# Kernel optimization log

Hardware: AMD Instinct MI355X
Metric: run time of the kernel (lower is better)

The kernel has to match this reference:

```python
import jax, jax.numpy as jnp
import numpy as np

B, S, E, H, D, F = 384, 128, 512, 4, 128, 2048

def setup_inputs() -> dict:
    key = jax.random.key(0)
    ks = jax.random.split(key, 13)
    lecun = lambda k, fan_in, shape: jax.random.normal(k, shape, jnp.float32) / jnp.sqrt(fan_in)
    return {
        "x": jax.random.normal(ks[0], (B, S, E), jnp.float32),
        "wq": lecun(ks[1], E, (E, E)), "bq": jnp.zeros((E,), jnp.float32),
        "wk": lecun(ks[2], E, (E, E)), "bk": jnp.zeros((E,), jnp.float32),
        "wv": lecun(ks[3], E, (E, E)), "bv": jnp.zeros((E,), jnp.float32),
        "wo": lecun(ks[4], E, (E, E)), "bo": jnp.zeros((E,), jnp.float32),
        "w1": lecun(ks[5], E, (E, F)), "b1": jnp.zeros((F,), jnp.float32),
        "w2": lecun(ks[6], F, (F, E)), "b2": jnp.zeros((E,), jnp.float32),
    }

def reference(x, wq, bq, wk, bk, wv, bv, wo, bo, w1, b1, w2, b2):
    # Attention (no 1/sqrt(d) scaling, no causal mask — matches source)
    q = (x @ wq + bq).reshape(B, S, H, D)
    k = (x @ wk + bk).reshape(B, S, H, D)
    v = (x @ wv + bv).reshape(B, S, H, D)
    scores = jnp.einsum('bshd,bthd->bhst', q, k)  # [B,H,S,S]
    weights = jax.nn.softmax(scores, axis=-1)
    attn = jnp.einsum('bhst,bthd->bshd', weights, v).reshape(B, S, E)
    x = x + (attn @ wo + bo)
    # MLP with residual
    h = jax.nn.relu(x @ w1 + b1)
    x = x + (h @ w2 + b2)
    return x
```

## Files before the change

kernel.cpp:

```cpp
#include <hip/hip_runtime.h>
#include <hip/hip_bf16.h>
#include <stdint.h>

typedef unsigned short u16;
typedef _Float16 f16;
typedef __attribute__((ext_vector_type(8))) f16 f16x8;
typedef __attribute__((ext_vector_type(4))) float f32x4;
typedef __attribute__((ext_vector_type(8))) u16 u16x8;

__device__ __forceinline__ u16 f2h(float f) {
    return __builtin_bit_cast(u16, (f16)f);
}
__device__ __forceinline__ float h2f(u16 u) {
    return (float)__builtin_bit_cast(f16, u);
}

#define GLDS16(g, l) __builtin_amdgcn_global_load_lds( \
    (const __attribute__((address_space(1))) void*)(uintptr_t)(g), \
    (__attribute__((address_space(3))) void*)(uintptr_t)(l), 16, 0, 0)

__global__ __launch_bounds__(256) void transpose_w(
    const float* __restrict__ in, u16* __restrict__ out,
    int K, int N, int rowOff)
{
    __shared__ float tile[32][33];
    int n0 = blockIdx.x * 32;
    int k0 = blockIdx.y * 32;
    int tx = threadIdx.x & 31;
    int ty = threadIdx.x >> 5;
#pragma unroll
    for (int i = 0; i < 4; ++i) {
        int k = ty + i * 8;
        tile[k][tx] = in[(size_t)(k0 + k) * N + n0 + tx];
    }
    __syncthreads();
#pragma unroll
    for (int i = 0; i < 4; ++i) {
        int n = ty + i * 8;
        out[(size_t)(rowOff + n0 + n) * K + k0 + tx] = f2h(tile[tx][n]);
    }
}

__global__ __launch_bounds__(256) void transpose_w4(
    const float* __restrict__ wq, const float* __restrict__ wk,
    const float* __restrict__ wv, const float* __restrict__ wo,
    u16* __restrict__ wqkvT, u16* __restrict__ woT)
{
    __shared__ float tile[32][33];
    const float* src[4] = {wq, wk, wv, wo};
    const int z = blockIdx.z;
    const float* in = src[z];
    u16* out = (z == 3) ? woT : (wqkvT + (size_t)z * 512 * 512);
    int n0 = blockIdx.x * 32;
    int k0 = blockIdx.y * 32;
    int tx = threadIdx.x & 31;
    int ty = threadIdx.x >> 5;
#pragma unroll
    for (int i = 0; i < 4; ++i) {
        int k = ty + i * 8;
        tile[k][tx] = in[(size_t)(k0 + k) * 512 + n0 + tx];
    }
    __syncthreads();
#pragma unroll
    for (int i = 0; i < 4; ++i) {
        int n = ty + i * 8;
        out[(size_t)(n0 + n) * 512 + k0 + tx] = f2h(tile[tx][n]);
    }
}

__global__ void pack_bias3(const float* __restrict__ bq, const float* __restrict__ bk,
                           const float* __restrict__ bv, float* __restrict__ bqkv)
{
    int i = blockIdx.x * 256 + threadIdx.x;
    float v;
    if (i < 512) v = bq[i];
    else if (i < 1024) v = bk[i - 512];
    else v = bv[i - 1024];
    bqkv[i] = v;
}

__global__ __launch_bounds__(256) void convert_x(const float* __restrict__ in,
                                                 u16* __restrict__ out)
{
    size_t i = ((size_t)blockIdx.x * 256 + threadIdx.x) * 8;
    float4 a = *(const float4*)(in + i);
    float4 b = *(const float4*)(in + i + 4);
    u16x8 r;
    r[0] = f2h(a.x); r[1] = f2h(a.y); r[2] = f2h(a.z); r[3] = f2h(a.w);
    r[4] = f2h(b.x); r[5] = f2h(b.y); r[6] = f2h(b.z); r[7] = f2h(b.w);
    *(u16x8*)(out + i) = r;
}

template<int RES, bool RELU, bool WH, bool WF32>
__global__ __launch_bounds__(256, 2) void gemm_bt(
    const u16* __restrict__ A, int lda,
    const u16* __restrict__ BT, int ldb,
    const float* __restrict__ bias, const float* __restrict__ res,
    u16* __restrict__ outh, float* __restrict__ outf,
    int nb_n, int N, int K)
{
    __shared__ u16 As[128 * 64];
    __shared__ u16 Bs[128 * 64];
    const int tid  = threadIdx.x;
    const int lane = tid & 63;
    const int wv   = tid >> 6;
    const int nwg  = gridDim.x;
    const int cpx  = nwg >> 3;
    const int logical = (blockIdx.x & 7) * cpx + (blockIdx.x >> 3);
    const int m0   = (logical / nb_n) * 128;
    const int n0   = (logical % nb_n) * 128;
    const int wm   = (wv >> 1) * 64;
    const int wn   = (wv & 1) * 64;
    const int lhi  = lane >> 4;
    const int llo  = lane & 15;

    f32x4 acc[4][4] = {};

    for (int kt = 0; kt < K; kt += 64) {
        __syncthreads();
#pragma unroll
        for (int i = 0; i < 4; ++i) {
            int c = i * 256 + tid;
            int row = c >> 3;
            int chunk = (c & 7) ^ (row & 7);
            const u16* ga = A  + (size_t)(m0 + row) * lda + kt + chunk * 8;
            const u16* gb = BT + (size_t)(n0 + row) * ldb + kt + chunk * 8;
            char* la = (char*)As + ((i * 256 + wv * 64) << 4);
            char* lb = (char*)Bs + ((i * 256 + wv * 64) << 4);
            GLDS16(ga, la);
            GLDS16(gb, lb);
        }
        __syncthreads();
#pragma unroll
        for (int fk = 0; fk < 2; ++fk) {
            f16x8 af[4], bfr[4];
#pragma unroll
            for (int f = 0; f < 4; ++f) {
                int ra = wm + f * 16 + llo;
                af[f] = *(const f16x8*)((const char*)As +
                        ((ra << 7) + ((fk * 64 + (lhi << 4)) ^ ((ra & 7) << 4))));
                int rb = wn + f * 16 + llo;
                bfr[f] = *(const f16x8*)((const char*)Bs +
                        ((rb << 7) + ((fk * 64 + (lhi << 4)) ^ ((rb & 7) << 4))));
            }
#pragma unroll
            for (int fm = 0; fm < 4; ++fm)
#pragma unroll
                for (int fn = 0; fn < 4; ++fn)
                    acc[fm][fn] = __builtin_amdgcn_mfma_f32_16x16x32_f16(
                        af[fm], bfr[fn], acc[fm][fn], 0, 0, 0);
        }
    }

    const int cr = lhi * 4;
#pragma unroll
    for (int fm = 0; fm < 4; ++fm) {
#pragma unroll
        for (int fn = 0; fn < 4; ++fn) {
            const int col = n0 + wn + fn * 16 + llo;
            const float bia = bias[col];
#pragma unroll
            for (int r = 0; r < 4; ++r) {
                const int row = m0 + wm + fm * 16 + cr + r;
                float v = acc[fm][fn][r] + bia;
                if constexpr (RES) v += res[(size_t)row * N + col];
                if constexpr (RELU) v = fmaxf(v, 0.f);
                if constexpr (WF32) outf[(size_t)row * N + col] = v;
                if constexpr (WH)   outh[(size_t)row * N + col] = f2h(v);
            }
        }
    }
}

__global__ __launch_bounds__(256, 2) void attn_kernel(
    const u16* __restrict__ qkv, u16* __restrict__ attn)
{
    __shared__ u16 VT[128 * 128];
    __shared__ u16 Plds[4 * 32 * 128];
    const int tid  = threadIdx.x;
    const int lane = tid & 63;
    const int wv   = tid >> 6;
    const int b    = blockIdx.x >> 2;
    const int hh   = blockIdx.x & 3;
    const int lhi  = lane >> 4;
    const int llo  = lane & 15;
    const u16* base = qkv + (size_t)b * 128 * 1536;

#pragma unroll
    for (int i = 0; i < 8; ++i) {
        int c = i * 256 + tid;
        int t = c >> 4;
        int ch = c & 15;
        uint4 raw = *(const uint4*)(base + (size_t)t * 1536 + 1024 + hh * 128 + ch * 8);
        const u16* e = (const u16*)&raw;
#pragma unroll
        for (int j = 0; j < 8; ++j) {
            int d = ch * 8 + j;
            *(u16*)((char*)VT + ((d << 8) + ((t * 2) ^ ((d & 7) << 4)))) = e[j];
        }
    }

    f16x8 qf[2][4];
#pragma unroll
    for (int fm = 0; fm < 2; ++fm)
#pragma unroll
        for (int fk = 0; fk < 4; ++fk) {
            int srow = wv * 32 + fm * 16 + llo;
            qf[fm][fk] = *(const f16x8*)(base + (size_t)srow * 1536 + hh * 128 + fk * 32 + lhi * 8);
        }

    f32x4 acc[2][8] = {};
#pragma unroll
    for (int ft = 0; ft < 8; ++ft) {
        f16x8 kf[4];
#pragma unroll
        for (int fk = 0; fk < 4; ++fk) {
            int trow = ft * 16 + llo;
            kf[fk] = *(const f16x8*)(base + (size_t)trow * 1536 + 512 + hh * 128 + fk * 32 + lhi * 8);
        }
#pragma unroll
        for (int fm = 0; fm < 2; ++fm)
#pragma unroll
            for (int fk = 0; fk < 4; ++fk)
                acc[fm][ft] = __builtin_amdgcn_mfma_f32_16x16x32_f16(
                    qf[fm][fk], kf[fk], acc[fm][ft], 0, 0, 0);
    }

    float inv[2][4];
#pragma unroll
    for (int fm = 0; fm < 2; ++fm)
#pragma unroll
        for (int r = 0; r < 4; ++r) {
            float mx = acc[fm][0][r];
#pragma unroll
            for (int ft = 1; ft < 8; ++ft) mx = fmaxf(mx, acc[fm][ft][r]);
            mx = fmaxf(mx, __shfl_xor(mx, 1, 64));
            mx = fmaxf(mx, __shfl_xor(mx, 2, 64));
            mx = fmaxf(mx, __shfl_xor(mx, 4, 64));
            mx = fmaxf(mx, __shfl_xor(mx, 8, 64));
            float s = 0.f;
#pragma unroll
            for (int ft = 0; ft < 8; ++ft) {
                float p = __expf(acc[fm][ft][r] - mx);
                acc[fm][ft][r] = p;
                s += p;
            }
            s += __shfl_xor(s, 1, 64);
            s += __shfl_xor(s, 2, 64);
            s += __shfl_xor(s, 4, 64);
            s += __shfl_xor(s, 8, 64);
            inv[fm][r] = 1.f / s;
        }

    char* Pw = (char*)Plds + wv * 8192;
#pragma unroll
    for (int fm = 0; fm < 2; ++fm)
#pragma unroll
        for (int ft = 0; ft < 8; ++ft)
#pragma unroll
            for (int r = 0; r < 4; ++r) {
                int m = fm * 16 + lhi * 4 + r;
                int t = ft * 16 + llo;
                *(u16*)(Pw + ((m << 8) + ((t * 2) ^ ((m & 7) << 4)))) = f2h(acc[fm][ft][r]);
            }

    __syncthreads();

    f16x8 pf[2][4];
#pragma unroll
    for (int fm = 0; fm < 2; ++fm)
#pragma unroll
        for (int k2 = 0; k2 < 4; ++k2) {
            int m = fm * 16 + llo;
            pf[fm][k2] = *(const f16x8*)(Pw +
                ((m << 8) + ((k2 * 64 + (lhi << 4)) ^ ((m & 7) << 4))));
        }

    f32x4 o[2][8] = {};
#pragma unroll
    for (int fd = 0; fd < 8; ++fd) {
        f16x8 vf[4];
#pragma unroll
        for (int k2 = 0; k2 < 4; ++k2) {
            int d = fd * 16 + llo;
            vf[k2] = *(const f16x8*)((const char*)VT +
                ((d << 8) + ((k2 * 64 + (lhi << 4)) ^ ((d & 7) << 4))));
        }
#pragma unroll
        for (int fm = 0; fm < 2; ++fm)
#pragma unroll
            for (int k2 = 0; k2 < 4; ++k2)
                o[fm][fd] = __builtin_amdgcn_mfma_f32_16x16x32_f16(
                    pf[fm][k2], vf[k2], o[fm][fd], 0, 0, 0);
    }

#pragma unroll
    for (int fm = 0; fm < 2; ++fm)
#pragma unroll
        for (int fd = 0; fd < 8; ++fd)
#pragma unroll
            for (int r = 0; r < 4; ++r) {
                int row = b * 128 + wv * 32 + fm * 16 + lhi * 4 + r;
                int col = hh * 128 + fd * 16 + llo;
                attn[(size_t)row * 512 + col] = f2h(o[fm][fd][r] * inv[fm][r]);
            }
}

extern "C" void kernel_launch(void* const* d_in, const int* in_sizes, int n_in,
                              void* d_out, int out_size, void* d_ws, size_t ws_size,
                              hipStream_t stream)
{
    const float* x  = (const float*)d_in[0];
    const float* wq = (const float*)d_in[1];
    const float* bq = (const float*)d_in[2];
    const float* wk = (const float*)d_in[3];
    const float* bk = (const float*)d_in[4];
    const float* wv = (const float*)d_in[5];
    const float* bv = (const float*)d_in[6];
    const float* wo = (const float*)d_in[7];
    const float* bo = (const float*)d_in[8];
    const float* w1 = (const float*)d_in[9];
    const float* b1 = (const float*)d_in[10];
    const float* w2 = (const float*)d_in[11];
    const float* b2 = (const float*)d_in[12];
    float* out = (float*)d_out;

    char* ws = (char*)d_ws;
    u16*   wqkvT = (u16*)(ws + 0);
    u16*   woT   = (u16*)(ws + 1572864);
    u16*   w1T   = (u16*)(ws + 2097152);
    u16*   w2T   = (u16*)(ws + 4194304);
    float* bqkv  = (float*)(ws + 6291456);
    u16*   xf    = (u16*)(ws + 6297600);
    u16*   qkv   = (u16*)(ws + 56629248);
    u16*   attno = xf;
    u16*   x1h   = qkv;
    u16*   hbuf  = (u16*)(ws + 106960896);
    float* x1f   = (float*)d_out;

    transpose_w4<<<dim3(16, 16, 4), 256, 0, stream>>>(wq, wk, wv, wo, wqkvT, woT);
    transpose_w<<<dim3(64, 16), 256, 0, stream>>>(w1, w1T, 512, 2048, 0);
    transpose_w<<<dim3(16, 64), 256, 0, stream>>>(w2, w2T, 2048, 512, 0);
    pack_bias3<<<6, 256, 0, stream>>>(bq, bk, bv, bqkv);
    convert_x<<<12288, 256, 0, stream>>>(x, xf);

    gemm_bt<0, false, true, false><<<4608, 256, 0, stream>>>(
        xf, 512, wqkvT, 512, bqkv, nullptr, qkv, nullptr, 12, 1536, 512);
    attn_kernel<<<1536, 256, 0, stream>>>(qkv, attno);
    gemm_bt<1, false, true, true><<<1536, 256, 0, stream>>>(
        attno, 512, woT, 512, bo, x, x1h, x1f, 4, 512, 512);
    gemm_bt<0, true, true, false><<<6144, 256, 0, stream>>>(
        x1h, 512, w1T, 512, b1, nullptr, hbuf, nullptr, 16, 2048, 512);
    gemm_bt<1, false, false, true><<<1536, 256, 0, stream>>>(
        hbuf, 2048, w2T, 2048, b2, x1f, nullptr, out, 4, 512, 2048);
}
```

Before: 512.9 us.

## Replace 128x128 GEMM with 256x256 eight-wave ping-pong pipelined GEMM

Swaps the 128x128-tile, 4-wave GEMM for a 256x256-tile, 8-wave kernel. It double-buffers A and B in 128KB of LDS and prefetches the next K-tiles with global_load_lds while MFMAs run on the current tile. The MFMA work is split into four quadrant phases, each with raised wave priority and explicit barriers and waitcnts, so LDS reads, global loads and matrix math interleave. Larger tiles improve operand reuse and cut global traffic. In exchange, occupancy drops to about one block per CU, the manual scheduling is fragile, and grids become small for the N=512 GEMMs (384 blocks).

```diff
diff --git a/kernel.cpp b/kernel.cpp
--- a/kernel.cpp
+++ b/kernel.cpp
@@ -11,13 +11,16 @@
 __device__ __forceinline__ u16 f2h(float f) {
     return __builtin_bit_cast(u16, (f16)f);
 }
-__device__ __forceinline__ float h2f(u16 u) {
-    return (float)__builtin_bit_cast(f16, u);
-}
 
 #define GLDS16(g, l) __builtin_amdgcn_global_load_lds( \
     (const __attribute__((address_space(1))) void*)(uintptr_t)(g), \
     (__attribute__((address_space(3))) void*)(uintptr_t)(l), 16, 0, 0)
+
+#define WAITL() do { asm volatile("s_waitcnt lgkmcnt(0)" ::: "memory"); \
+                     __builtin_amdgcn_sched_barrier(0); } while (0)
+#define BARR()  do { __builtin_amdgcn_sched_barrier(0); \
+                     __builtin_amdgcn_s_barrier(); \
+                     __builtin_amdgcn_sched_barrier(0); } while (0)
 
 __global__ __launch_bounds__(256) void transpose_w(
     const float* __restrict__ in, u16* __restrict__ out,
@@ -91,78 +94,149 @@
     *(u16x8*)(out + i) = r;
 }
 
+template<int MG, int NG>
+__device__ __forceinline__ void mmaQ(f32x4 (&acc)[8][4], const f16x8 (&a)[4][2],
+                                     const f16x8 (&bb)[2][2])
+{
+    __builtin_amdgcn_s_setprio(1);
+#pragma unroll
+    for (int ks = 0; ks < 2; ++ks)
+#pragma unroll
+        for (int mf = 0; mf < 4; ++mf)
+#pragma unroll
+            for (int nf = 0; nf < 2; ++nf)
+                acc[MG * 4 + mf][NG * 2 + nf] = __builtin_amdgcn_mfma_f32_16x16x32_f16(
+                    a[mf][ks], bb[nf][ks], acc[MG * 4 + mf][NG * 2 + nf], 0, 0, 0);
+    __builtin_amdgcn_s_setprio(0);
+}
+
 template<int RES, bool RELU, bool WH, bool WF32>
-__global__ __launch_bounds__(256, 2) void gemm_bt(
+__global__ __launch_bounds__(512, 2) void gemm256(
     const u16* __restrict__ A, int lda,
     const u16* __restrict__ BT, int ldb,
     const float* __restrict__ bias, const float* __restrict__ res,
     u16* __restrict__ outh, float* __restrict__ outf,
     int nb_n, int N, int K)
 {
-    __shared__ u16 As[128 * 64];
-    __shared__ u16 Bs[128 * 64];
+    __shared__ u16 lds[65536];
+    char* ldsc = (char*)lds;
     const int tid  = threadIdx.x;
     const int lane = tid & 63;
-    const int wv   = tid >> 6;
+    const int w    = tid >> 6;
+    const int wm   = w >> 2;
+    const int wn   = w & 3;
+    const int lhi  = lane >> 4;
+    const int llo  = lane & 15;
     const int nwg  = gridDim.x;
     const int cpx  = nwg >> 3;
     const int logical = (blockIdx.x & 7) * cpx + (blockIdx.x >> 3);
-    const int m0   = (logical / nb_n) * 128;
-    const int n0   = (logical % nb_n) * 128;
-    const int wm   = (wv >> 1) * 64;
-    const int wn   = (wv & 1) * 64;
-    const int lhi  = lane >> 4;
-    const int llo  = lane & 15;
-
-    f32x4 acc[4][4] = {};
-
-    for (int kt = 0; kt < K; kt += 64) {
-        __syncthreads();
-#pragma unroll
-        for (int i = 0; i < 4; ++i) {
-            int c = i * 256 + tid;
-            int row = c >> 3;
-            int chunk = (c & 7) ^ (row & 7);
-            const u16* ga = A  + (size_t)(m0 + row) * lda + kt + chunk * 8;
-            const u16* gb = BT + (size_t)(n0 + row) * ldb + kt + chunk * 8;
-            char* la = (char*)As + ((i * 256 + wv * 64) << 4);
-            char* lb = (char*)Bs + ((i * 256 + wv * 64) << 4);
-            GLDS16(ga, la);
-            GLDS16(gb, lb);
-        }
-        __syncthreads();
-#pragma unroll
-        for (int fk = 0; fk < 2; ++fk) {
-            f16x8 af[4], bfr[4];
-#pragma unroll
-            for (int f = 0; f < 4; ++f) {
-                int ra = wm + f * 16 + llo;
-                af[f] = *(const f16x8*)((const char*)As +
-                        ((ra << 7) + ((fk * 64 + (lhi << 4)) ^ ((ra & 7) << 4))));
-                int rb = wn + f * 16 + llo;
-                bfr[f] = *(const f16x8*)((const char*)Bs +
-                        ((rb << 7) + ((fk * 64 + (lhi << 4)) ^ ((rb & 7) << 4))));
-            }
-#pragma unroll
-            for (int fm = 0; fm < 4; ++fm)
-#pragma unroll
-                for (int fn = 0; fn < 4; ++fn)
-                    acc[fm][fn] = __builtin_amdgcn_mfma_f32_16x16x32_f16(
-                        af[fm], bfr[fn], acc[fm][fn], 0, 0, 0);
-        }
-    }
-
-    const int cr = lhi * 4;
-#pragma unroll
-    for (int fm = 0; fm < 4; ++fm) {
-#pragma unroll
-        for (int fn = 0; fn < 4; ++fn) {
-            const int col = n0 + wn + fn * 16 + llo;
+    const int m0   = (logical / nb_n) * 256;
+    const int n0   = (logical % nb_n) * 256;
+    const int nt   = K >> 6;
+
+    const int sx    = (llo & 7) << 4;
+    const int koff0 = (lhi * 16) ^ sx;
+    const int koff1 = (64 + lhi * 16) ^ sx;
+    const int arow  = (wm * 128 + llo) * 128;
+    const int brow  = (wn * 64 + llo) * 128;
+
+    f32x4 acc[8][4] = {};
+    f16x8 aF[4][2], bF0[2][2], bF1[2][2];
+
+    auto stgA = [&](int b, int h, int kt) {
+#pragma unroll
+        for (int j = 0; j < 2; ++j) {
+            int c = j * 512 + w * 64 + lane;
+            int r = c >> 3;
+            int ch = (c & 7) ^ (r & 7);
+            const u16* g = A + (size_t)(m0 + h * 128 + r) * lda + kt + ch * 8;
+            char* l = ldsc + b * 65536 + h * 16384 + ((j * 512 + w * 64) << 4);
+            GLDS16(g, l);
+        }
+    };
+    auto stgB = [&](int b, int h, int kt) {
+#pragma unroll
+        for (int j = 0; j < 2; ++j) {
+            int c = j * 512 + w * 64 + lane;
+            int r = c >> 3;
+            int ch = (c & 7) ^ (r & 7);
+            const u16* g = BT + (size_t)(n0 + h * 128 + r) * ldb + kt + ch * 8;
+            char* l = ldsc + b * 65536 + 32768 + h * 16384 + ((j * 512 + w * 64) << 4);
+            GLDS16(g, l);
+        }
+    };
+    auto rdA = [&](int b, int mf, int ks) -> f16x8 {
+        return *(const f16x8*)(ldsc + b * 65536 + arow + mf * 2048
+                               + (ks ? koff1 : koff0));
+    };
+    auto rdB = [&](int b, int nf, int ks) -> f16x8 {
+        return *(const f16x8*)(ldsc + b * 65536 + 32768 + brow + nf * 2048
+                               + (ks ? koff1 : koff0));
+    };
+
+    stgA(0, 0, 0); stgA(0, 1, 0);
+    stgB(0, 0, 0); stgB(0, 1, 0);
+    stgB(1, 0, 64); stgB(1, 1, 64);
+    asm volatile("s_waitcnt vmcnt(4)" ::: "memory");
+    BARR();
+
+    for (int t = 0; t < nt; ++t) {
+        const int b = t & 1;
+        int t1 = t + 1; if (t1 >= nt) t1 -= nt;
+        int t2 = t + 2; if (t2 >= nt) t2 -= nt;
+
+#pragma unroll
+        for (int mf = 0; mf < 4; ++mf) {
+            aF[mf][0] = rdA(b, mf, 0); aF[mf][1] = rdA(b, mf, 1);
+        }
+#pragma unroll
+        for (int nf = 0; nf < 2; ++nf) {
+            bF0[nf][0] = rdB(b, nf, 0); bF0[nf][1] = rdB(b, nf, 1);
+        }
+        stgA(b ^ 1, 0, t1 << 6);
+        __builtin_amdgcn_s_barrier();
+        WAITL();
+        mmaQ<0, 0>(acc, aF, bF0);
+        BARR();
+
+#pragma unroll
+        for (int nf = 0; nf < 2; ++nf) {
+            bF1[nf][0] = rdB(b, nf + 2, 0); bF1[nf][1] = rdB(b, nf + 2, 1);
+        }
+        stgA(b ^ 1, 1, t1 << 6);
+        __builtin_amdgcn_s_barrier();
+        WAITL();
+        mmaQ<0, 1>(acc, aF, bF1);
+        BARR();
+
+#pragma unroll
+        for (int mf = 0; mf < 4; ++mf) {
+            aF[mf][0] = rdA(b, mf + 4, 0); aF[mf][1] = rdA(b, mf + 4, 1);
+        }
+        stgB(b, 0, t2 << 6);
+        __builtin_amdgcn_s_barrier();
+        WAITL();
+        mmaQ<1, 0>(acc, aF, bF0);
+        BARR();
+
+        stgB(b, 1, t2 << 6);
+        __builtin_amdgcn_s_barrier();
+        __builtin_amdgcn_sched_barrier(0);
+        mmaQ<1, 1>(acc, aF, bF1);
+        asm volatile("s_waitcnt vmcnt(4)" ::: "memory");
+        BARR();
+    }
+
+#pragma unroll
+    for (int mf = 0; mf < 8; ++mf) {
+#pragma unroll
+        for (int nf = 0; nf < 4; ++nf) {
+            const int col = n0 + wn * 64 + nf * 16 + llo;
             const float bia = bias[col];
 #pragma unroll
             for (int r = 0; r < 4; ++r) {
-                const int row = m0 + wm + fm * 16 + cr + r;
-                float v = acc[fm][fn][r] + bia;
+                const int row = m0 + wm * 128 + mf * 16 + lhi * 4 + r;
+                float v = acc[mf][nf][r] + bia;
                 if constexpr (RES) v += res[(size_t)row * N + col];
                 if constexpr (RELU) v = fmaxf(v, 0.f);
                 if constexpr (WF32) outf[(size_t)row * N + col] = v;
@@ -344,13 +418,13 @@
     pack_bias3<<<6, 256, 0, stream>>>(bq, bk, bv, bqkv);
     convert_x<<<12288, 256, 0, stream>>>(x, xf);
 
-    gemm_bt<0, false, true, false><<<4608, 256, 0, stream>>>(
-        xf, 512, wqkvT, 512, bqkv, nullptr, qkv, nullptr, 12, 1536, 512);
+    gemm256<0, false, true, false><<<1152, 512, 0, stream>>>(
+        xf, 512, wqkvT, 512, bqkv, nullptr, qkv, nullptr, 6, 1536, 512);
     attn_kernel<<<1536, 256, 0, stream>>>(qkv, attno);
-    gemm_bt<1, false, true, true><<<1536, 256, 0, stream>>>(
-        attno, 512, woT, 512, bo, x, x1h, x1f, 4, 512, 512);
-    gemm_bt<0, true, true, false><<<6144, 256, 0, stream>>>(
-        x1h, 512, w1T, 512, b1, nullptr, hbuf, nullptr, 16, 2048, 512);
-    gemm_bt<1, false, false, true><<<1536, 256, 0, stream>>>(
-        hbuf, 2048, w2T, 2048, b2, x1f, nullptr, out, 4, 512, 2048);
-}
+    gemm256<1, false, true, true><<<384, 512, 0, stream>>>(
+        attno, 512, woT, 512, bo, x, x1h, x1f, 2, 512, 512);
+    gemm256<0, true, true, false><<<1536, 512, 0, stream>>>(
+        x1h, 512, w1T, 512, b1, nullptr, hbuf, nullptr, 8, 2048, 512);
+    gemm256<1, false, false, true><<<384, 512, 0, stream>>>(
+        hbuf, 2048, w2T, 2048, b2, x1f, nullptr, out, 2, 512, 2048);
+}
```

Measured after the change: 553.7 us. 7.9% more time.
